# Kernel optimization log

Hardware: AMD Instinct MI355X
Metric: run time of the kernel (lower is better)

Reference implementation:

```python
import jax, jax.numpy as jnp
import numpy as np

VOCAB, N_CLASS, H, E = 50000, 6, 512, 300
B, S = 256, 512


def setup_inputs() -> dict:
    key = jax.random.key(0)
    ks = jax.random.split(key, 10)
    return {
        "seq": jax.random.randint(ks[0], (B, S), 0, VOCAB),
        "classes": jnp.arange(N_CLASS),
        "embed_W": jax.random.normal(ks[1], (VOCAB, E), jnp.float32) * 0.1,
        "embed_class_W": jax.random.normal(ks[2], (N_CLASS, H), jnp.float32) * 0.1,
        "W_ih": jax.random.normal(ks[3], (3 * H, E), jnp.float32) * 0.05,
        "W_hh": jax.random.normal(ks[4], (3 * H, H), jnp.float32) * 0.05,
        "b_ih": jax.random.normal(ks[5], (3 * H,), jnp.float32) * 0.05,
        "b_hh": jax.random.normal(ks[6], (3 * H,), jnp.float32) * 0.05,
        "attend": jax.random.normal(ks[7], (H, H), jnp.float32) * 0.1,
        "W_cls": jax.random.normal(ks[8], (2, H), jnp.float32) * 0.05,
        "b_cls": jax.random.normal(ks[9], (2,), jnp.float32) * 0.05,
    }


def _gru_scan(xs, W_ih, W_hh, b_ih, b_hh):
    # xs: [S, B, E]; torch GRUCell semantics
    h0 = jnp.zeros((xs.shape[1], W_hh.shape[1]), xs.dtype)

    def step(h, x):
        gi = x @ W_ih.T + b_ih            # [B, 3H]
        gh = h @ W_hh.T + b_hh            # [B, 3H]
        i_r, i_z, i_n = jnp.split(gi, 3, axis=-1)
        h_r, h_z, h_n = jnp.split(gh, 3, axis=-1)
        r = jax.nn.sigmoid(i_r + h_r)
        z = jax.nn.sigmoid(i_z + h_z)
        n = jnp.tanh(i_n + r * h_n)
        h_new = (1.0 - z) * n + z * h
        return h_new, h_new

    _, hs = jax.lax.scan(step, h0, xs)
    return hs  # [S, B, H]


def reference(seq, classes, embed_W, embed_class_W, W_ih, W_hh, b_ih, b_hh,
              attend, W_cls, b_cls):
    pad_mask = (seq > 0).astype(embed_W.dtype)          # [B, S]
    seq_emb = jnp.tanh(embed_W[seq])                    # [B, S, E]
    hs = _gru_scan(seq_emb.transpose(1, 0, 2), W_ih, W_hh, b_ih, b_hh)
    seq_repr = hs.transpose(1, 0, 2)                    # [B, S, H]

    class_emb = embed_class_W[classes]                  # [C, H]
    attn = jnp.tanh(class_emb) @ attend                 # [C, H]
    # scores[c,b,s] = tanh(attn)[c] . seq_repr[b,s], masked
    scores = jnp.einsum('ch,bsh->cbs', jnp.tanh(attn), seq_repr)
    scores = scores * pad_mask[None, :, :]
    ctx = jnp.einsum('cbs,bsh->cbh', jnp.tanh(scores), seq_repr)  # [C, B, H]
    logits = jnp.tanh(ctx) @ W_cls.T + b_cls            # [C, B, 2]
    return jax.nn.log_softmax(logits, axis=-1)
```

## Files before the change

### kernel.cpp

```cpp
#include <hip/hip_runtime.h>
#include <cstdint>
#include <cstddef>

#define NB 256
#define NS 512
#define NE 300
#define NH 512

using f32x4 = __attribute__((ext_vector_type(4))) float;
using s16x8 = __attribute__((ext_vector_type(8))) short;

static __device__ __forceinline__ unsigned short f2bf(float f) {
  unsigned u = __float_as_uint(f);
  u += 0x7FFFu + ((u >> 16) & 1u);
  return (unsigned short)(u >> 16);
}
static __device__ __forceinline__ float bf2f(unsigned short h) {
  return __uint_as_float(((unsigned)h) << 16);
}
static __device__ __forceinline__ float fast_tanh(float x) {
  float xc = fminf(fmaxf(x, -9.f), 9.f);
  float e = __expf(2.f * xc);
  return (e - 1.f) / (e + 1.f);
}
static __device__ __forceinline__ float sigm(float x) {
  return 1.f / (1.f + __expf(-x));
}

__global__ void k_zero(unsigned short* __restrict__ h_ex, unsigned* __restrict__ cnt) {
  int i = blockIdx.x * 256 + threadIdx.x;
  f32x4 z = {0.f, 0.f, 0.f, 0.f};
  *(f32x4*)(h_ex + (size_t)i * 16) = z;
  *(f32x4*)(h_ex + (size_t)i * 16 + 8) = z;
  if (i < 512) cnt[i] = 0;
}

__global__ __launch_bounds__(256) void k_amat(const int* __restrict__ classes,
                                              const float* __restrict__ ecw,
                                              const float* __restrict__ attend,
                                              unsigned short* __restrict__ a_bf) {
  __shared__ float tc[6][512];
  const int tid = threadIdx.x, j = blockIdx.x;
  for (int i = tid; i < 6 * 512; i += 256) {
    int c = i >> 9, hp = i & 511;
    tc[c][hp] = fast_tanh(ecw[(size_t)classes[c] * 512 + hp]);
  }
  __syncthreads();
  #pragma unroll
  for (int i = 0; i < 4; ++i) {
    int task = tid + 256 * i;
    int c = task >> 6, hl = task & 63;
    int h = j * 64 + hl;
    float v = 0.f;
    if (c < 6) {
      float acc = 0.f;
      for (int hp = 0; hp < 512; ++hp) acc += tc[c][hp] * attend[(size_t)hp * 512 + h];
      v = fast_tanh(acc);
    }
    a_bf[c * 512 + h] = f2bf(v);
  }
}

__global__ __launch_bounds__(384) void k_gru(
    const int* __restrict__ seq, const float* __restrict__ embed_W,
    const float* __restrict__ W_ih, const float* __restrict__ W_hh,
    const float* __restrict__ b_ih, const float* __restrict__ b_hh,
    unsigned short* __restrict__ h_ex, unsigned* __restrict__ cnt,
    unsigned short* __restrict__ seq_repr)
{
  __shared__ unsigned short x_lds[2][16][328];
  __shared__ unsigned short h_lds[16][520];
  __shared__ float rz_lds[2][16][32];

  const int tid = threadIdx.x;
  const int w = tid >> 6, l = tid & 63, lo = l & 15, hi = l >> 4;
  const int bid = blockIdx.x;
  const int g_b = (bid & 7) * 2 + (bid >> 7);
  const int g_c = (bid >> 3) & 15;

  const int gg = w >> 1;
  const int cb = (w & 1) * 16;
  const int jrow = gg * 512 + g_c * 32 + cb + lo;

  s16x8 whh[16];
  #pragma unroll
  for (int kt = 0; kt < 16; ++kt) {
    const float* p = W_hh + (size_t)jrow * 512 + kt * 32 + hi * 8;
    f32x4 a0 = *(const f32x4*)p;
    f32x4 a1 = *(const f32x4*)(p + 4);
    s16x8 v;
    v[0]=(short)f2bf(a0[0]); v[1]=(short)f2bf(a0[1]); v[2]=(short)f2bf(a0[2]); v[3]=(short)f2bf(a0[3]);
    v[4]=(short)f2bf(a1[0]); v[5]=(short)f2bf(a1[1]); v[6]=(short)f2bf(a1[2]); v[7]=(short)f2bf(a1[3]);
    whh[kt] = v;
  }
  s16x8 wih[10];
  #pragma unroll
  for (int kt = 0; kt < 10; ++kt) {
    s16x8 v;
    #pragma unroll
    for (int jj = 0; jj < 8; ++jj) {
      int k = kt * 32 + hi * 8 + jj;
      float f = (k < NE) ? W_ih[(size_t)jrow * NE + k] : 0.f;
      v[jj] = (short)f2bf(f);
    }
    wih[kt] = v;
  }
  const float bsum = b_ih[jrow] + b_hh[jrow];
  const float bni = b_ih[jrow], bnh = b_hh[jrow];

  float hcar[4] = {0.f, 0.f, 0.f, 0.f};
  unsigned* mycnt = cnt + g_b * 32;

  auto do_gather = [&](int ss) {
    const int buf = ss & 1;
    #pragma unroll
    for (int i = 0; i < 2; ++i) {
      int task = tid + 384 * i;
      if (task < 640) {
        int r = task & 15, grp = task >> 4;
        float vals[8];
        if (grp < 38) {
          int id = seq[(size_t)(g_b * 16 + r) * NS + ss];
          const float* ep = embed_W + (size_t)id * NE;
          if (grp < 37) {
            f32x4 u0 = *(const f32x4*)(ep + grp * 8);
            f32x4 u1 = *(const f32x4*)(ep + grp * 8 + 4);
            vals[0]=u0[0];vals[1]=u0[1];vals[2]=u0[2];vals[3]=u0[3];
            vals[4]=u1[0];vals[5]=u1[1];vals[6]=u1[2];vals[7]=u1[3];
          } else {
            #pragma unroll
            for (int jj = 0; jj < 8; ++jj) { int cc = 296 + jj; vals[jj] = (cc < NE) ? ep[cc] : 0.f; }
          }
        } else {
          #pragma unroll
          for (int jj = 0; jj < 8; ++jj) vals[jj] = 0.f;
        }
        s16x8 pv;
        #pragma unroll
        for (int jj = 0; jj < 8; ++jj) pv[jj] = (short)f2bf(fast_tanh(vals[jj]));
        *(s16x8*)&x_lds[buf][r][grp * 8] = pv;
      }
    }
  };

  do_gather(0);
  __syncthreads();

  #pragma unroll 1
  for (int s = 0; s < NS; ++s) {
    if (s + 1 < NS) do_gather(s + 1);

    f32x4 ax = {0.f,0.f,0.f,0.f};
    #pragma unroll
    for (int kt = 0; kt < 10; ++kt) {
      s16x8 af = *(const s16x8*)&x_lds[s & 1][lo][kt * 32 + hi * 8];
      ax = __builtin_amdgcn_mfma_f32_16x16x32_bf16(af, wih[kt], ax, 0, 0, 0);
    }

    if (tid == 0 && s > 0) {
      unsigned target = 32u * (unsigned)s;
      int guard = 0;
      while (__hip_atomic_load(mycnt, __ATOMIC_RELAXED, __HIP_MEMORY_SCOPE_AGENT) < target) {
        __builtin_amdgcn_s_sleep(1);
        if (++guard > (1 << 26)) break;
      }
    }
    __syncthreads();

    const unsigned short* hsrc = h_ex + ((size_t)(s & 1) * 16 + g_b) * (16 * 512);
    #pragma unroll
    for (int i = 0; i < 6; ++i) {
      int task = tid + 384 * i;
      if (task < 2048) {
        int r = task >> 7, c8 = task & 127;
        unsigned long long v = __hip_atomic_load(
            (const unsigned long long*)(hsrc + r * 512 + c8 * 4),
            __ATOMIC_RELAXED, __HIP_MEMORY_SCOPE_AGENT);
        *(unsigned long long*)&h_lds[r][c8 * 4] = v;
      }
    }
    __syncthreads();

    f32x4 ah = {0.f,0.f,0.f,0.f};
    #pragma unroll
    for (int kt = 0; kt < 16; ++kt) {
      s16x8 af = *(const s16x8*)&h_lds[lo][kt * 32 + hi * 8];
      ah = __builtin_amdgcn_mfma_f32_16x16x32_bf16(af, whh[kt], ah, 0, 0, 0);
    }

    if (w < 4) {
      #pragma unroll
      for (int j = 0; j < 4; ++j) {
        int row = hi * 4 + j;
        rz_lds[gg][row][cb + lo] = ax[j] + ah[j] + bsum;
      }
    }
    __syncthreads();

    if (w >= 4) {
      unsigned short* hdst = h_ex + ((size_t)((s + 1) & 1) * 16 + g_b) * (16 * 512);
      const int cpr = cb + lo;
      #pragma unroll
      for (int j = 0; j < 4; ++j) {
        int row = hi * 4 + j;
        float rr = sigm(rz_lds[0][row][cpr]);
        float zz = sigm(rz_lds[1][row][cpr]);
        float nn = fast_tanh(ax[j] + bni + rr * (ah[j] + bnh));
        float hn = (1.f - zz) * nn + zz * hcar[j];
        hcar[j] = hn;
        unsigned myb = (unsigned)f2bf(hn);
        unsigned other = __shfl_xor(myb, 1);
        if ((lo & 1) == 0) {
          unsigned word = myb | (other << 16);
          int col = g_c * 32 + cpr;
          __hip_atomic_store((unsigned*)(hdst + row * 512 + col), word,
                             __ATOMIC_RELAXED, __HIP_MEMORY_SCOPE_AGENT);
          *(unsigned*)(seq_repr + ((size_t)(g_b * 16 + row) * NS + s) * NH + col) = word;
        }
      }
      asm volatile("s_waitcnt vmcnt(0)" ::: "memory");
      if (l == 0)
        __hip_atomic_fetch_add(mycnt, 1u, __ATOMIC_RELAXED, __HIP_MEMORY_SCOPE_AGENT);
    }
  }
}

__global__ __launch_bounds__(256) void k_attn(const int* __restrict__ seq,
                                              const unsigned short* __restrict__ seq_repr,
                                              const unsigned short* __restrict__ a_bf,
                                              const float* __restrict__ W_cls,
                                              const float* __restrict__ b_cls,
                                              float* __restrict__ out)
{
  __shared__ unsigned short V[32][520];
  __shared__ float P[32][8];
  __shared__ float red[4][12];
  const int tid = threadIdx.x, b = blockIdx.x;
  const int w = tid >> 6, l = tid & 63, lo = l & 15, hi = l >> 4;

  s16x8 afr[16];
  #pragma unroll
  for (int kt = 0; kt < 16; ++kt)
    afr[kt] = *(const s16x8*)(a_bf + (size_t)lo * 512 + kt * 32 + hi * 8);

  float ctx0[6] = {0,0,0,0,0,0}, ctx1[6] = {0,0,0,0,0,0};
  const unsigned short* vbase = seq_repr + (size_t)b * NS * NH;

  for (int sc = 0; sc < 16; ++sc) {
    #pragma unroll 4
    for (int i = 0; i < 8; ++i) {
      int task = tid + 256 * i;
      int sl = task >> 6, grp = task & 63;
      s16x8 v = *(const s16x8*)(vbase + (size_t)(sc * 32 + sl) * NH + grp * 8);
      *(s16x8*)&V[sl][grp * 8] = v;
    }
    __syncthreads();
    if (w < 2) {
      f32x4 acc = {0.f,0.f,0.f,0.f};
      int sl0 = w * 16;
      #pragma unroll
      for (int kt = 0; kt < 16; ++kt) {
        s16x8 af = *(const s16x8*)&V[sl0 + lo][kt * 32 + hi * 8];
        acc = __builtin_amdgcn_mfma_f32_16x16x32_bf16(af, afr[kt], acc, 0, 0, 0);
      }
      if (lo < 8) {
        #pragma unroll
        for (int j = 0; j < 4; ++j) {
          int sl = sl0 + hi * 4 + j;
          float p = 0.f;
          if (lo < 6) {
            int s = sc * 32 + sl;
            p = (seq[(size_t)b * NS + s] > 0) ? fast_tanh(acc[j]) : 0.f;
          }
          P[sl][lo] = p;
        }
      }
    }
    __syncthreads();
    #pragma unroll 2
    for (int sl = 0; sl < 32; ++sl) {
      unsigned v2 = *(const unsigned*)&V[sl][tid * 2];
      float v0 = bf2f((unsigned short)(v2 & 0xFFFFu));
      float v1 = bf2f((unsigned short)(v2 >> 16));
      #pragma unroll
      for (int c = 0; c < 6; ++c) {
        float p = P[sl][c];
        ctx0[c] += p * v0; ctx1[c] += p * v1;
      }
    }
    __syncthreads();
  }

  float pl[12];
  #pragma unroll
  for (int c = 0; c < 6; ++c) {
    float t0 = fast_tanh(ctx0[c]), t1 = fast_tanh(ctx1[c]);
    pl[c * 2 + 0] = t0 * W_cls[tid * 2] + t1 * W_cls[tid * 2 + 1];
    pl[c * 2 + 1] = t0 * W_cls[512 + tid * 2] + t1 * W_cls[512 + tid * 2 + 1];
  }
  #pragma unroll
  for (int i = 0; i < 12; ++i) {
    float v = pl[i];
    for (int off = 32; off > 0; off >>= 1) v += __shfl_down(v, off);
    if (l == 0) red[w][i] = v;
  }
  __syncthreads();
  if (tid < 6) {
    int c = tid;
    float l0 = red[0][c*2] + red[1][c*2] + red[2][c*2] + red[3][c*2] + b_cls[0];
    float l1 = red[0][c*2+1] + red[1][c*2+1] + red[2][c*2+1] + red[3][c*2+1] + b_cls[1];
    float m = fmaxf(l0, l1);
    float lse = m + logf(__expf(l0 - m) + __expf(l1 - m));
    out[c * 512 + b * 2 + 0] = l0 - lse;
    out[c * 512 + b * 2 + 1] = l1 - lse;
  }
}

extern "C" void kernel_launch(void* const* d_in, const int* in_sizes, int n_in,
                              void* d_out, int out_size, void* d_ws, size_t ws_size,
                              hipStream_t stream) {
  const int*   seq      = (const int*)d_in[0];
  const int*   classes  = (const int*)d_in[1];
  const float* embed_W  = (const float*)d_in[2];
  const float* ecw      = (const float*)d_in[3];
  const float* W_ih     = (const float*)d_in[4];
  const float* W_hh     = (const float*)d_in[5];
  const float* b_ih     = (const float*)d_in[6];
  const float* b_hh     = (const float*)d_in[7];
  const float* attend   = (const float*)d_in[8];
  const float* W_cls    = (const float*)d_in[9];
  const float* b_cls    = (const float*)d_in[10];
  float* out = (float*)d_out;

  char* ws = (char*)d_ws;
  unsigned short* seq_repr = (unsigned short*)ws;
  unsigned short* h_ex     = (unsigned short*)(ws + 134217728);
  unsigned*       cnt      = (unsigned*)(ws + 134217728 + 524288);
  unsigned short* a_bf     = (unsigned short*)(ws + 134217728 + 524288 + 2048);

  hipLaunchKernelGGL(k_zero, dim3(64), dim3(256), 0, stream, h_ex, cnt);
  hipLaunchKernelGGL(k_amat, dim3(8), dim3(256), 0, stream, classes, ecw, attend, a_bf);
  hipLaunchKernelGGL(k_gru, dim3(256), dim3(384), 0, stream,
                     seq, embed_W, W_ih, W_hh, b_ih, b_hh, h_ex, cnt, seq_repr);
  hipLaunchKernelGGL(k_attn, dim3(256), dim3(256), 0, stream,
                     seq, seq_repr, a_bf, W_cls, b_cls, out);
}
```

Measured before the change: 2.429 ms.

## Replace shared atomic counter with per-block step flags polled by every thread

Replaces the per-batch-group atomic counter, which a single thread spun on, with per-producer-block flags storing the last completed step. Every thread now polls only the flag of the block that produces the hidden-state chunk it loads, so the barrier before the h load is dropped. The seq_repr store is moved after the waitcnt so only the exchange stores sit on the critical path, and the hh MFMA chain is split into two accumulators for more instruction-level parallelism. The risks are heavier polling traffic and the flag being set by tid 0 after a block barrier with only relaxed ordering, so visibility depends on the earlier waitcnt.

Result: slower. 3.610 ms (+48.6%).

```diff
diff --git a/kernel.cpp b/kernel.cpp
--- a/kernel.cpp
+++ b/kernel.cpp
@@ -27,12 +27,12 @@
   return 1.f / (1.f + __expf(-x));
 }
 
-__global__ void k_zero(unsigned short* __restrict__ h_ex, unsigned* __restrict__ cnt) {
+__global__ void k_zero(unsigned short* __restrict__ h_ex, unsigned* __restrict__ flags) {
   int i = blockIdx.x * 256 + threadIdx.x;
   f32x4 z = {0.f, 0.f, 0.f, 0.f};
   *(f32x4*)(h_ex + (size_t)i * 16) = z;
   *(f32x4*)(h_ex + (size_t)i * 16 + 8) = z;
-  if (i < 512) cnt[i] = 0;
+  if (i < 512) flags[i] = 0;
 }
 
 __global__ __launch_bounds__(256) void k_amat(const int* __restrict__ classes,
@@ -65,7 +65,7 @@
     const int* __restrict__ seq, const float* __restrict__ embed_W,
     const float* __restrict__ W_ih, const float* __restrict__ W_hh,
     const float* __restrict__ b_ih, const float* __restrict__ b_hh,
-    unsigned short* __restrict__ h_ex, unsigned* __restrict__ cnt,
+    unsigned short* __restrict__ h_ex, unsigned* __restrict__ flags,
     unsigned short* __restrict__ seq_repr)
 {
   __shared__ unsigned short x_lds[2][16][328];
@@ -109,7 +109,7 @@
   const float bni = b_ih[jrow], bnh = b_hh[jrow];
 
   float hcar[4] = {0.f, 0.f, 0.f, 0.f};
-  unsigned* mycnt = cnt + g_b * 32;
+  const unsigned* flg = flags + g_b * 16;
 
   auto do_gather = [&](int ss) {
     const int buf = ss & 1;
@@ -157,36 +157,47 @@
       ax = __builtin_amdgcn_mfma_f32_16x16x32_bf16(af, wih[kt], ax, 0, 0, 0);
     }
 
-    if (tid == 0 && s > 0) {
-      unsigned target = 32u * (unsigned)s;
+    if (s > 0) {
       int guard = 0;
-      while (__hip_atomic_load(mycnt, __ATOMIC_RELAXED, __HIP_MEMORY_SCOPE_AGENT) < target) {
+      for (;;) {
+        bool ok = true;
+        #pragma unroll
+        for (int i = 0; i < 6; ++i) {
+          int task = tid + 384 * i;
+          if (task < 2048) {
+            unsigned f = __hip_atomic_load(flg + ((task & 127) >> 3),
+                                           __ATOMIC_RELAXED, __HIP_MEMORY_SCOPE_AGENT);
+            ok &= (f >= (unsigned)s);
+          }
+        }
+        if (ok) break;
         __builtin_amdgcn_s_sleep(1);
-        if (++guard > (1 << 26)) break;
-      }
-    }
-    __syncthreads();
-
+        if (++guard > (1 << 24)) break;
+      }
+    }
     const unsigned short* hsrc = h_ex + ((size_t)(s & 1) * 16 + g_b) * (16 * 512);
     #pragma unroll
     for (int i = 0; i < 6; ++i) {
       int task = tid + 384 * i;
       if (task < 2048) {
-        int r = task >> 7, c8 = task & 127;
+        int r = task >> 7, c4 = task & 127;
         unsigned long long v = __hip_atomic_load(
-            (const unsigned long long*)(hsrc + r * 512 + c8 * 4),
+            (const unsigned long long*)(hsrc + r * 512 + c4 * 4),
             __ATOMIC_RELAXED, __HIP_MEMORY_SCOPE_AGENT);
-        *(unsigned long long*)&h_lds[r][c8 * 4] = v;
-      }
-    }
-    __syncthreads();
-
-    f32x4 ah = {0.f,0.f,0.f,0.f};
-    #pragma unroll
-    for (int kt = 0; kt < 16; ++kt) {
-      s16x8 af = *(const s16x8*)&h_lds[lo][kt * 32 + hi * 8];
-      ah = __builtin_amdgcn_mfma_f32_16x16x32_bf16(af, whh[kt], ah, 0, 0, 0);
-    }
+        *(unsigned long long*)&h_lds[r][c4 * 4] = v;
+      }
+    }
+    __syncthreads();
+
+    f32x4 ah0 = {0.f,0.f,0.f,0.f}, ah1 = {0.f,0.f,0.f,0.f};
+    #pragma unroll
+    for (int kt = 0; kt < 16; kt += 2) {
+      s16x8 af0 = *(const s16x8*)&h_lds[lo][kt * 32 + hi * 8];
+      s16x8 af1 = *(const s16x8*)&h_lds[lo][(kt + 1) * 32 + hi * 8];
+      ah0 = __builtin_amdgcn_mfma_f32_16x16x32_bf16(af0, whh[kt], ah0, 0, 0, 0);
+      ah1 = __builtin_amdgcn_mfma_f32_16x16x32_bf16(af1, whh[kt + 1], ah1, 0, 0, 0);
+    }
+    f32x4 ah = ah0 + ah1;
 
     if (w < 4) {
       #pragma unroll
@@ -200,6 +211,8 @@
     if (w >= 4) {
       unsigned short* hdst = h_ex + ((size_t)((s + 1) & 1) * 16 + g_b) * (16 * 512);
       const int cpr = cb + lo;
+      const int col = g_c * 32 + cpr;
+      unsigned words[4];
       #pragma unroll
       for (int j = 0; j < 4; ++j) {
         int row = hi * 4 + j;
@@ -210,18 +223,25 @@
         hcar[j] = hn;
         unsigned myb = (unsigned)f2bf(hn);
         unsigned other = __shfl_xor(myb, 1);
-        if ((lo & 1) == 0) {
-          unsigned word = myb | (other << 16);
-          int col = g_c * 32 + cpr;
-          __hip_atomic_store((unsigned*)(hdst + row * 512 + col), word,
+        words[j] = myb | (other << 16);
+      }
+      if ((lo & 1) == 0) {
+        #pragma unroll
+        for (int j = 0; j < 4; ++j)
+          __hip_atomic_store((unsigned*)(hdst + (hi * 4 + j) * 512 + col), words[j],
                              __ATOMIC_RELAXED, __HIP_MEMORY_SCOPE_AGENT);
-          *(unsigned*)(seq_repr + ((size_t)(g_b * 16 + row) * NS + s) * NH + col) = word;
-        }
       }
       asm volatile("s_waitcnt vmcnt(0)" ::: "memory");
-      if (l == 0)
-        __hip_atomic_fetch_add(mycnt, 1u, __ATOMIC_RELAXED, __HIP_MEMORY_SCOPE_AGENT);
-    }
+      if ((lo & 1) == 0) {
+        #pragma unroll
+        for (int j = 0; j < 4; ++j)
+          *(unsigned*)(seq_repr + ((size_t)(g_b * 16 + hi * 4 + j) * NS + s) * NH + col) = words[j];
+      }
+    }
+    __syncthreads();
+    if (tid == 0)
+      __hip_atomic_store((unsigned*)(flags + g_b * 16 + g_c), (unsigned)(s + 1),
+                         __ATOMIC_RELAXED, __HIP_MEMORY_SCOPE_AGENT);
   }
 }
 
@@ -335,13 +355,13 @@
   char* ws = (char*)d_ws;
   unsigned short* seq_repr = (unsigned short*)ws;
   unsigned short* h_ex     = (unsigned short*)(ws + 134217728);
-  unsigned*       cnt      = (unsigned*)(ws + 134217728 + 524288);
+  unsigned*       flags    = (unsigned*)(ws + 134217728 + 524288);
   unsigned short* a_bf     = (unsigned short*)(ws + 134217728 + 524288 + 2048);
 
-  hipLaunchKernelGGL(k_zero, dim3(64), dim3(256), 0, stream, h_ex, cnt);
+  hipLaunchKernelGGL(k_zero, dim3(64), dim3(256), 0, stream, h_ex, flags);
   hipLaunchKernelGGL(k_amat, dim3(8), dim3(256), 0, stream, classes, ecw, attend, a_bf);
   hipLaunchKernelGGL(k_gru, dim3(256), dim3(384), 0, stream,
-                     seq, embed_W, W_ih, W_hh, b_ih, b_hh, h_ex, cnt, seq_repr);
+                     seq, embed_W, W_ih, W_hh, b_ih, b_hh, h_ex, flags, seq_repr);
   hipLaunchKernelGGL(k_attn, dim3(256), dim3(256), 0, stream,
                      seq, seq_repr, a_bf, W_cls, b_cls, out);
 }
```
